# Kernel tuning notes

Measured on AMD Instinct MI355X. Metric: run time of the kernel, lower is better.

## Reference

```python
import jax, jax.numpy as jnp
import numpy as np
from jax import lax

D_MODEL, D_STATE, D_CONV, EXPAND = 1024, 16, 4, 2
D_INNER = EXPAND * D_MODEL
B, L = 2, 2048


def setup_inputs() -> dict:
    key = jax.random.key(0)
    ks = jax.random.split(key, 8)
    s_in = 1.0 / np.sqrt(D_MODEL)
    s_xp = 1.0 / np.sqrt(D_INNER)
    x = jax.random.normal(ks[0], (B, L, D_MODEL), dtype=jnp.float32)
    W_in = jax.random.uniform(ks[1], (2 * D_INNER, D_MODEL), minval=-s_in, maxval=s_in)
    conv_w = jax.random.uniform(ks[2], (D_INNER, 1, D_CONV), minval=-0.5, maxval=0.5)
    conv_b = jax.random.uniform(ks[3], (D_INNER,), minval=-0.5, maxval=0.5)
    W_xproj = jax.random.uniform(ks[4], (1 + 2 * D_STATE, D_INNER), minval=-s_xp, maxval=s_xp)
    W_dt = jax.random.uniform(ks[5], (D_INNER, 1), minval=-1.0, maxval=1.0)
    b_dt = jax.random.uniform(ks[6], (D_INNER,), minval=-1.0, maxval=1.0)
    A_log = jnp.log(jnp.broadcast_to(jnp.arange(1, D_STATE + 1, dtype=jnp.float32), (D_INNER, D_STATE)))
    D = jnp.ones((D_INNER,), dtype=jnp.float32)
    W_out = jax.random.uniform(ks[7], (D_MODEL, D_INNER), minval=-s_xp, maxval=s_xp)
    return {"x": x, "W_in": W_in, "conv_w": conv_w, "conv_b": conv_b,
            "W_xproj": W_xproj, "W_dt": W_dt, "b_dt": b_dt,
            "A_log": A_log, "D": D, "W_out": W_out}


def reference(x, W_in, conv_w, conv_b, W_xproj, W_dt, b_dt, A_log, D, W_out):
    b, l, _ = x.shape
    d_state = A_log.shape[1]
    d_conv = conv_w.shape[-1]

    xz = x @ W_in.T                                  # (B, L, 2*d_inner)
    x_in, z = jnp.split(xz, 2, axis=-1)

    # causal depthwise conv: torch pads both sides then truncates to [:L]
    lhs = jnp.pad(x_in.transpose(0, 2, 1), ((0, 0), (0, 0), (d_conv - 1, 0)))  # (B, d_inner, L+pad)
    conv = lax.conv_general_dilated(
        lhs, conv_w, window_strides=(1,), padding='VALID',
        dimension_numbers=('NCW', 'OIW', 'NCW'),
        feature_group_count=conv_w.shape[0])
    x_conv = jax.nn.silu(conv.transpose(0, 2, 1) + conv_b)  # (B, L, d_inner)

    ssm_in = x_conv @ W_xproj.T                      # (B, L, 1+2*d_state)
    dt_raw = ssm_in[..., :1]
    B_ssm = ssm_in[..., 1:1 + d_state]               # (B, L, d_state)
    C_ssm = ssm_in[..., 1 + d_state:]                # (B, L, d_state)

    delta = jax.nn.softplus(dt_raw @ W_dt.T + b_dt)  # (B, L, d_inner)
    A = -jnp.exp(A_log)                              # (d_inner, d_state)
    deltaA = jnp.exp(delta[..., None] * A)           # (B, L, d_inner, d_state)
    deltaB_u = delta[..., None] * B_ssm[:, :, None, :] * x_conv[..., None]

    def step(h, inp):
        dA, dBu, c = inp                              # (B,d_inner,d_state)x2, (B,d_state)
        h = dA * h + dBu
        y = jnp.einsum('bds,bs->bd', h, c)
        return h, y

    h0 = jnp.zeros((b, deltaA.shape[2], d_state), dtype=x.dtype)
    _, ys = lax.scan(step, h0, (deltaA.transpose(1, 0, 2, 3),
                                deltaB_u.transpose(1, 0, 2, 3),
                                C_ssm.transpose(1, 0, 2)))
    y = ys.transpose(1, 0, 2) + x_conv * D           # (B, L, d_inner)
    y = y * jax.nn.silu(z)
    return y @ W_out.T
```

## Files before the change

kernel.cpp:

```cpp
#include <hip/hip_runtime.h>
#include <hip/hip_bf16.h>
#include <math.h>

#define D_MODEL 1024
#define D_STATE 16
#define D_CONV  4
#define D_INNER 2048
#define BB      2
#define LL      2048
#define BLROWS  (BB*LL)
#define SSML    36
#define XSPLIT  16

typedef __hip_bfloat16 bf16;
typedef __attribute__((ext_vector_type(8))) short short8;
typedef __attribute__((ext_vector_type(4))) float f32x4;

__device__ __forceinline__ float ldf(const void* p, long i, int isbf) {
    return isbf ? __bfloat162float(((const bf16*)p)[i]) : ((const float*)p)[i];
}
__device__ __forceinline__ short bfbits(float f) {
    bf16 h = __float2bfloat16(f);
    return *(short*)&h;
}
__device__ __forceinline__ float bits2f(short s) {
    bf16 h; *(short*)&h = s; return __bfloat162float(h);
}
__device__ __forceinline__ float bf2f(bf16 h) { return __bfloat162float(h); }
__device__ __forceinline__ float siluf(float x) {
    return __fdividef(x, 1.f + __expf(-x));
}
__device__ __forceinline__ void softplus_r(float x, float& delta, float& r) {
    float e = __expf(-fabsf(x));
    float t = 1.f + e;
    delta = fmaxf(x, 0.f) + __logf(t);
    r = __fdividef((x >= 0.f) ? e : 1.f, t);
}
__device__ __forceinline__ void pow16(float r, float* p) {
    p[0]=r;        p[1]=r*r;      p[2]=p[1]*r;    p[3]=p[1]*p[1];
    p[4]=p[3]*p[0];p[5]=p[3]*p[1];p[6]=p[3]*p[2]; p[7]=p[3]*p[3];
    p[8]=p[7]*p[0];p[9]=p[7]*p[1];p[10]=p[7]*p[2];p[11]=p[7]*p[3];
    p[12]=p[7]*p[4];p[13]=p[7]*p[5];p[14]=p[7]*p[6];p[15]=p[7]*p[7];
}

#define OFF_CW   0
#define OFF_CB   8192
#define OFF_WDT  10240
#define OFF_BDT  12288
#define OFF_AA   14336
#define OFF_D    47104
#define N_SMALL  49152
#define N_WXPB   (128*2048)
#define N_SSMZ   (BLROWS*SSML)

__global__ void dtype_probe(const unsigned short* __restrict__ alog, int* __restrict__ flag) {
    if (threadIdx.x == 0) { flag[0] = (alog[1] != 0) ? 1 : 0; flag[1] = 1; }
}

__global__ __launch_bounds__(256) void cvt_prep(
    const void* __restrict__ Wxp, const void* __restrict__ cw,
    const void* __restrict__ cb, const void* __restrict__ wdt,
    const void* __restrict__ bdt, const void* __restrict__ alog,
    const void* __restrict__ Dp,
    bf16* __restrict__ wxpb, float* __restrict__ smallf,
    float* __restrict__ ssm, int* __restrict__ flag)
{
    const int isbf = flag[0];
    int idx = blockIdx.x * 256 + threadIdx.x;
    if (idx < N_WXPB) {
        int row = idx >> 11, col = idx & 2047;
        float v = (row < 33) ? ldf(Wxp, (long)row*2048 + col, isbf) : 0.f;
        wxpb[idx] = __float2bfloat16(v);
        return;
    }
    int j = idx - N_WXPB;
    if      (j < 8192)  smallf[OFF_CW  + j]         = ldf(cw,  j, isbf);
    else if (j < 10240) smallf[OFF_CB  + j - 8192]  = ldf(cb,  j - 8192, isbf);
    else if (j < 12288) smallf[OFF_WDT + j - 10240] = ldf(wdt, j - 10240, isbf);
    else if (j < 14336) smallf[OFF_BDT + j - 12288] = ldf(bdt, j - 12288, isbf);
    else if (j < 47104) {
        int jj = j - 14336;
        float aa = -__expf(ldf(alog, jj, isbf));
        smallf[OFF_AA + jj] = aa;
        int s = jj & 15;
        if (fabsf(aa + (float)(s+1)) > 1e-3f) flag[1] = 0;
    }
    else if (j < 49152) smallf[OFF_D   + j - 47104] = ldf(Dp,  j - 47104, isbf);
    else {
        int z = j - N_SMALL;
        if (z < N_SSMZ) ssm[z] = 0.f;
    }
}

__global__ __launch_bounds__(256) void cvt_all(
    const void* __restrict__ x, const void* __restrict__ win,
    const void* __restrict__ wout,
    bf16* __restrict__ xb, bf16* __restrict__ winb, bf16* __restrict__ woutb,
    const int* __restrict__ flagp)
{
    const int isbf = *flagp;
    int i = blockIdx.x * 256 + threadIdx.x;
    const void* src; bf16* dst; long o;
    if (i < 524288)       { src = x;    dst = xb;    o = (long)i * 8; }
    else if (i < 1048576) { src = win;  dst = winb;  o = (long)(i - 524288) * 8; }
    else if (i < 1310720) { src = wout; dst = woutb; o = (long)(i - 1048576) * 8; }
    else return;
    short8 v;
    if (isbf) {
        v = *(const short8*)((const bf16*)src + o);
    } else {
        const float* s = (const float*)src + o;
        f32x4 u = *(const f32x4*)s, w = *(const f32x4*)(s + 4);
        v[0]=bfbits(u[0]); v[1]=bfbits(u[1]); v[2]=bfbits(u[2]); v[3]=bfbits(u[3]);
        v[4]=bfbits(w[0]); v[5]=bfbits(w[1]); v[6]=bfbits(w[2]); v[7]=bfbits(w[3]);
    }
    *(short8*)(dst + o) = v;
}

__global__ __launch_bounds__(256) void gemm_dual(
    const void* __restrict__ A, int lda,
    const void* __restrict__ Bm, int ldb,
    void* __restrict__ Cp, int ldc, int K,
    const int* __restrict__ flagp, int amode, int bmode, int cmode)
{
    const int isbf = *flagp;
    const int a_bf = amode ? isbf : 1;
    const int b_bf = bmode ? isbf : 1;
    const int c_bf = cmode ? isbf : 1;

    __shared__ bf16 As[128*64];
    __shared__ bf16 Bs[128*64];
    const int t    = threadIdx.x;
    const int lane = t & 63;
    const int w    = t >> 6;
    const int wm   = w >> 1, wn = w & 1;
    const int bm   = blockIdx.y, bn = blockIdx.x;
    const int quad = lane >> 4, l16 = lane & 15;

    f32x4 acc[4][4];
    #pragma unroll
    for (int i = 0; i < 4; i++)
        #pragma unroll
        for (int j = 0; j < 4; j++)
            acc[i][j] = f32x4{0.f, 0.f, 0.f, 0.f};

    for (int k0 = 0; k0 < K; k0 += 64) {
        __syncthreads();
        if (a_bf) {
            #pragma unroll
            for (int seg = 0; seg < 4; seg++) {
                int s = seg*256 + t, row = s >> 3, sg = s & 7;
                int col = (sg ^ (row & 7)) * 8;
                const bf16* ga = (const bf16*)A + ((long)bm*128 + row)*(long)lda + k0 + col;
                __builtin_amdgcn_global_load_lds(
                    (const __attribute__((address_space(1))) void*)ga,
                    (__attribute__((address_space(3))) void*)&As[row*64 + sg*8], 16, 0, 0);
            }
        } else {
            #pragma unroll
            for (int seg = 0; seg < 4; seg++) {
                int s = seg*256 + t, row = s >> 3, sg = s & 7;
                int col = (sg ^ (row & 7)) * 8;
                const float* ap = (const float*)A + ((long)bm*128 + row)*(long)lda + k0 + col;
                f32x4 u = *(const f32x4*)ap, v = *(const f32x4*)(ap + 4);
                short8 va;
                va[0]=bfbits(u[0]); va[1]=bfbits(u[1]); va[2]=bfbits(u[2]); va[3]=bfbits(u[3]);
                va[4]=bfbits(v[0]); va[5]=bfbits(v[1]); va[6]=bfbits(v[2]); va[7]=bfbits(v[3]);
                *(short8*)&As[row*64 + sg*8] = va;
            }
        }
        if (b_bf) {
            #pragma unroll
            for (int seg = 0; seg < 4; seg++) {
                int s = seg*256 + t, row = s >> 3, sg = s & 7;
                int col = (sg ^ (row & 7)) * 8;
                const bf16* gb = (const bf16*)Bm + ((long)bn*128 + row)*(long)ldb + k0 + col;
                __builtin_amdgcn_global_load_lds(
                    (const __attribute__((address_space(1))) void*)gb,
                    (__attribute__((address_space(3))) void*)&Bs[row*64 + sg*8], 16, 0, 0);
            }
        } else {
            #pragma unroll
            for (int seg = 0; seg < 4; seg++) {
                int s = seg*256 + t, row = s >> 3, sg = s & 7;
                int col = (sg ^ (row & 7)) * 8;
                const float* bp = (const float*)Bm + ((long)bn*128 + row)*(long)ldb + k0 + col;
                f32x4 u = *(const f32x4*)bp, v = *(const f32x4*)(bp + 4);
                short8 vb;
                vb[0]=bfbits(u[0]); vb[1]=bfbits(u[1]); vb[2]=bfbits(u[2]); vb[3]=bfbits(u[3]);
                vb[4]=bfbits(v[0]); vb[5]=bfbits(v[1]); vb[6]=bfbits(v[2]); vb[7]=bfbits(v[3]);
                *(short8*)&Bs[row*64 + sg*8] = vb;
            }
        }
        __syncthreads();

        #pragma unroll
        for (int kk = 0; kk < 64; kk += 32) {
            const int cbase = kk >> 3;
            short8 af[4], bfr[4];
            #pragma unroll
            for (int mi = 0; mi < 4; mi++) {
                int row = wm*64 + mi*16 + l16;
                int c = cbase + quad;
                af[mi] = *(const short8*)&As[row*64 + ((c ^ (row & 7))*8)];
            }
            #pragma unroll
            for (int ni = 0; ni < 4; ni++) {
                int row = wn*64 + ni*16 + l16;
                int c = cbase + quad;
                bfr[ni] = *(const short8*)&Bs[row*64 + ((c ^ (row & 7))*8)];
            }
            #pragma unroll
            for (int mi = 0; mi < 4; mi++)
                #pragma unroll
                for (int ni = 0; ni < 4; ni++)
                    acc[mi][ni] = __builtin_amdgcn_mfma_f32_16x16x32_bf16(
                        af[mi], bfr[ni], acc[mi][ni], 0, 0, 0);
        }
    }

    #pragma unroll
    for (int mi = 0; mi < 4; mi++)
        #pragma unroll
        for (int ni = 0; ni < 4; ni++)
            #pragma unroll
            for (int r = 0; r < 4; r++) {
                int row = bm*128 + wm*64 + mi*16 + quad*4 + r;
                int col = bn*128 + wn*64 + ni*16 + l16;
                float val = acc[mi][ni][r];
                if (c_bf) ((bf16*)Cp)[(long)row * ldc + col] = __float2bfloat16(val);
                else      ((float*)Cp)[(long)row * ldc + col] = val;
            }
}

__global__ __launch_bounds__(256) void gemm_n64(
    const bf16* __restrict__ A, int lda,
    const void* __restrict__ Bm, int ldb,
    void* __restrict__ Cp, int ldc, int K,
    const int* __restrict__ flagp, int bmode, int cmode)
{
    const int isbf = *flagp;
    const int b_bf = bmode ? isbf : 1;
    const int c_bf = cmode ? isbf : 1;

    __shared__ bf16 As[128*64];
    __shared__ bf16 Bs[64*64];
    const int t    = threadIdx.x;
    const int lane = t & 63;
    const int w    = t >> 6;
    const int wm   = w >> 1, wn = w & 1;
    const int bm   = blockIdx.y, bn = blockIdx.x;
    const int quad = lane >> 4, l16 = lane & 15;

    f32x4 acc[4][2];
    #pragma unroll
    for (int i = 0; i < 4; i++)
        #pragma unroll
        for (int j = 0; j < 2; j++)
            acc[i][j] = f32x4{0.f, 0.f, 0.f, 0.f};

    for (int k0 = 0; k0 < K; k0 += 64) {
        __syncthreads();
        #pragma unroll
        for (int seg = 0; seg < 4; seg++) {
            int s = seg*256 + t, row = s >> 3, sg = s & 7;
            int col = (sg ^ (row & 7)) * 8;
            const bf16* ga = A + ((long)bm*128 + row)*(long)lda + k0 + col;
            __builtin_amdgcn_global_load_lds(
                (const __attribute__((address_space(1))) void*)ga,
                (__attribute__((address_space(3))) void*)&As[row*64 + sg*8], 16, 0, 0);
        }
        if (b_bf) {
            #pragma unroll
            for (int seg = 0; seg < 2; seg++) {
                int s = seg*256 + t, row = s >> 3, sg = s & 7;
                int col = (sg ^ (row & 7)) * 8;
                const bf16* gb = (const bf16*)Bm + ((long)bn*64 + row)*(long)ldb + k0 + col;
                __builtin_amdgcn_global_load_lds(
                    (const __attribute__((address_space(1))) void*)gb,
                    (__attribute__((address_space(3))) void*)&Bs[row*64 + sg*8], 16, 0, 0);
            }
        } else {
            #pragma unroll
            for (int seg = 0; seg < 2; seg++) {
                int s = seg*256 + t, row = s >> 3, sg = s & 7;
                int col = (sg ^ (row & 7)) * 8;
                const float* bp = (const float*)Bm + ((long)bn*64 + row)*(long)ldb + k0 + col;
                f32x4 u = *(const f32x4*)bp, v = *(const f32x4*)(bp + 4);
                short8 vb;
                vb[0]=bfbits(u[0]); vb[1]=bfbits(u[1]); vb[2]=bfbits(u[2]); vb[3]=bfbits(u[3]);
                vb[4]=bfbits(v[0]); vb[5]=bfbits(v[1]); vb[6]=bfbits(v[2]); vb[7]=bfbits(v[3]);
                *(short8*)&Bs[row*64 + sg*8] = vb;
            }
        }
        __syncthreads();

        #pragma unroll
        for (int kk = 0; kk < 64; kk += 32) {
            const int cbase = kk >> 3;
            short8 af[4], bfr[2];
            #pragma unroll
            for (int mi = 0; mi < 4; mi++) {
                int row = wm*64 + mi*16 + l16;
                int c = cbase + quad;
                af[mi] = *(const short8*)&As[row*64 + ((c ^ (row & 7))*8)];
            }
            #pragma unroll
            for (int ni = 0; ni < 2; ni++) {
                int row = wn*32 + ni*16 + l16;
                int c = cbase + quad;
                bfr[ni] = *(const short8*)&Bs[row*64 + ((c ^ (row & 7))*8)];
            }
            #pragma unroll
            for (int mi = 0; mi < 4; mi++)
                #pragma unroll
                for (int ni = 0; ni < 2; ni++)
                    acc[mi][ni] = __builtin_amdgcn_mfma_f32_16x16x32_bf16(
                        af[mi], bfr[ni], acc[mi][ni], 0, 0, 0);
        }
    }

    #pragma unroll
    for (int mi = 0; mi < 4; mi++)
        #pragma unroll
        for (int ni = 0; ni < 2; ni++)
            #pragma unroll
            for (int r = 0; r < 4; r++) {
                int row = bm*128 + wm*64 + mi*16 + quad*4 + r;
                int col = bn*64 + wn*32 + ni*16 + l16;
                float val = acc[mi][ni][r];
                if (c_bf) ((bf16*)Cp)[(long)row * ldc + col] = __float2bfloat16(val);
                else      ((float*)Cp)[(long)row * ldc + col] = val;
            }
}

__global__ __launch_bounds__(256) void xproj_fused(
    const bf16* __restrict__ xz, const bf16* __restrict__ wxpb,
    const float* __restrict__ smallf, float* __restrict__ ssm)
{
    const float* cwf = smallf + OFF_CW;
    const float* cbf = smallf + OFF_CB;
    __shared__ bf16 As[128*32];
    __shared__ bf16 Bs[128*32];
    const int t    = threadIdx.x;
    const int lane = t & 63;
    const int w    = t >> 6;
    const int wm   = w >> 1, wn = w & 1;
    const int bm   = blockIdx.y;
    const int ks   = blockIdx.x * (D_INNER / XSPLIT);
    const int quad = lane >> 4, l16 = lane & 15;

    f32x4 acc[4][4];
    #pragma unroll
    for (int i = 0; i < 4; i++)
        #pragma unroll
        for (int j = 0; j < 4; j++)
            acc[i][j] = f32x4{0.f, 0.f, 0.f, 0.f};

    for (int k0 = ks; k0 < ks + D_INNER/XSPLIT; k0 += 32) {
        __syncthreads();
        #pragma unroll
        for (int seg = 0; seg < 2; seg++) {
            int s = seg*256 + t, row = s >> 2, dcol = (s & 3) * 8;
            int blg = bm*128 + row;
            int b = blg >> 11, l = blg & (LL - 1);
            int d0 = k0 + dcol;
            float a[8];
            {
                f32x4 c0 = *(const f32x4*)&cbf[d0], c1 = *(const f32x4*)&cbf[d0+4];
                a[0]=c0[0]; a[1]=c0[1]; a[2]=c0[2]; a[3]=c0[3];
                a[4]=c1[0]; a[5]=c1[1]; a[6]=c1[2]; a[7]=c1[3];
            }
            f32x4 cw4[8];
            #pragma unroll
            for (int j = 0; j < 8; j++) cw4[j] = *(const f32x4*)&cwf[(d0+j)*4];
            #pragma unroll
            for (int kk = 0; kk < D_CONV; kk++) {
                int ls = l - 3 + kk;
                if (ls >= 0) {
                    short8 xv = *(const short8*)&xz[((long)(b*LL + ls))*4096 + d0];
                    #pragma unroll
                    for (int j = 0; j < 8; j++) a[j] += bits2f(xv[j]) * cw4[j][kk];
                }
            }
            short8 va;
            #pragma unroll
            for (int j = 0; j < 8; j++) va[j] = bfbits(siluf(a[j]));
            *(short8*)&As[row*32 + dcol] = va;
        }
        #pragma unroll
        for (int seg = 0; seg < 2; seg++) {
            int s = seg*256 + t, row = s >> 2, col = (s & 3) * 8;
            const bf16* gb = wxpb + (long)row*D_INNER + k0 + col;
            __builtin_amdgcn_global_load_lds(
                (const __attribute__((address_space(1))) void*)gb,
                (__attribute__((address_space(3))) void*)&Bs[row*32 + col], 16, 0, 0);
        }
        __syncthreads();

        short8 af[4], bfr[4];
        #pragma unroll
        for (int mi = 0; mi < 4; mi++)
            af[mi] = *(const short8*)&As[(wm*64 + mi*16 + l16)*32 + quad*8];
        #pragma unroll
        for (int ni = 0; ni < 4; ni++)
            bfr[ni] = *(const short8*)&Bs[(wn*64 + ni*16 + l16)*32 + quad*8];
        #pragma unroll
        for (int mi = 0; mi < 4; mi++)
            #pragma unroll
            for (int ni = 0; ni < 4; ni++)
                acc[mi][ni] = __builtin_amdgcn_mfma_f32_16x16x32_bf16(
                    af[mi], bfr[ni], acc[mi][ni], 0, 0, 0);
    }

    #pragma unroll
    for (int mi = 0; mi < 4; mi++)
        #pragma unroll
        for (int ni = 0; ni < 4; ni++) {
            int col = wn*64 + ni*16 + l16;
            if (col < 33) {
                int newcol = (col == 0) ? 32 : (col - 1);
                #pragma unroll
                for (int r = 0; r < 4; r++) {
                    int row = bm*128 + wm*64 + mi*16 + quad*4 + r;
                    atomicAdd(&ssm[(long)row * SSML + newcol], acc[mi][ni][r]);
                }
            }
        }
}

template<int CHUNK_T>
__global__ __launch_bounds__(256) void scan_partA(
    const float* __restrict__ ssm, const bf16* __restrict__ xz,
    const float* __restrict__ smallf,
    float* __restrict__ sumdq, float* __restrict__ Q,
    const int* __restrict__ flag)
{
    __shared__ float sL[CHUNK_T*SSML];
    __shared__ bf16  sX[CHUNK_T*256];
    const int fastA = flag[1];
    int d = blockIdx.x * 256 + threadIdx.x;
    int c = blockIdx.y, b = blockIdx.z;
    const int NC = gridDim.y;
    int l0 = c * CHUNK_T;
    {
        const float* src = ssm + (long)(b*LL + l0) * SSML;
        for (int idx = threadIdx.x; idx < CHUNK_T*SSML; idx += 256) sL[idx] = src[idx];
        const bf16* xsrc = xz + (long)(b*LL + l0)*4096 + blockIdx.x*256;
        for (int j = threadIdx.x; j < CHUNK_T*32; j += 256) {
            int li = j >> 5, ln = j & 31;
            *(short8*)&sX[li*256 + ln*8] = *(const short8*)&xsrc[(long)li*4096 + ln*8];
        }
    }
    float h[D_STATE];
    #pragma unroll
    for (int s = 0; s < D_STATE; s++) h[s] = 0.f;
    float Aa[D_STATE];
    if (!fastA) {
        #pragma unroll
        for (int s = 0; s < D_STATE; s++) Aa[s] = smallf[OFF_AA + d*D_STATE + s];
    }
    f32x4 cw4 = *(const f32x4*)&smallf[OFF_CW + d*4];
    float cbv  = smallf[OFF_CB + d];
    float wdt  = smallf[OFF_WDT + d];
    float bdtv = smallf[OFF_BDT + d];
    float win[3];
    #pragma unroll
    for (int k = 0; k < 3; k++) {
        int ls = l0 - 3 + k;
        win[k] = (ls >= 0) ? bf2f(xz[((long)(b*LL + ls))*4096 + d]) : 0.f;
    }
    __syncthreads();
    float sumd = 0.f;
    #pragma unroll 4
    for (int li = 0; li < CHUNK_T; li++) {
        float xnew = bf2f(sX[li*256 + threadIdx.x]);
        float convv = cbv + win[0]*cw4[0] + win[1]*cw4[1] + win[2]*cw4[2] + xnew*cw4[3];
        win[0] = win[1]; win[1] = win[2]; win[2] = xnew;
        float xc = siluf(convv);
        const float* row = &sL[li*SSML];
        f32x4 Bv[4];
        #pragma unroll
        for (int g = 0; g < 4; g++) Bv[g] = *(const f32x4*)(row + g*4);
        float delta, r;
        softplus_r(row[32]*wdt + bdtv, delta, r);
        sumd += delta;
        float du = delta * xc;
        if (fastA) {
            float p[16];
            pow16(r, p);
            #pragma unroll
            for (int g = 0; g < 4; g++)
                #pragma unroll
                for (int j = 0; j < 4; j++) {
                    int s = g*4 + j;
                    h[s] = p[s]*h[s] + du*Bv[g][j];
                }
        } else {
            #pragma unroll
            for (int g = 0; g < 4; g++)
                #pragma unroll
                for (int j = 0; j < 4; j++) {
                    int s = g*4 + j;
                    h[s] = __expf(delta*Aa[s])*h[s] + du*Bv[g][j];
                }
        }
    }
    sumdq[(long)(b*NC + c)*D_INNER + d] = sumd;
    long o = ((long)(b*NC + c)*D_STATE)*D_INNER + d;
    #pragma unroll
    for (int s = 0; s < D_STATE; s++)
        Q[o + (long)s*D_INNER] = h[s];
}

__global__ __launch_bounds__(256) void scan_combine(
    const float* __restrict__ sumdq, float* __restrict__ Q_hst,
    const float* __restrict__ smallf, int NC)
{
    int t = blockIdx.x * 256 + threadIdx.x;
    int d = t & (D_INNER - 1);
    int s = (t >> 11) & (D_STATE - 1);
    int b = t >> 15;
    float Aa = smallf[OFF_AA + d*D_STATE + s];
    float h = 0.f;
    #pragma unroll 4
    for (int c = 0; c < NC; c++) {
        float sd = sumdq[(long)(b*NC + c)*D_INNER + d];
        long idx = ((long)(b*NC + c)*D_STATE + s)*D_INNER + d;
        float q = Q_hst[idx];
        Q_hst[idx] = h;
        h = __expf(Aa*sd)*h + q;
    }
}

template<int CHUNK_T>
__global__ __launch_bounds__(256) void scan_partC(
    const float* __restrict__ ssm, bf16* __restrict__ xz,
    const float* __restrict__ smallf, const float* __restrict__ hst,
    const int* __restrict__ flag)
{
    __shared__ float sL[CHUNK_T*SSML];
    __shared__ bf16  sX[CHUNK_T*256];
    __shared__ bf16  sZ[CHUNK_T*256];
    const int fastA = flag[1];
    int d = blockIdx.x * 256 + threadIdx.x;
    int c = blockIdx.y, b = blockIdx.z;
    const int NC = gridDim.y;
    int l0 = c * CHUNK_T;
    {
        const float* src = ssm + (long)(b*LL + l0) * SSML;
        for (int idx = threadIdx.x; idx < CHUNK_T*SSML; idx += 256) sL[idx] = src[idx];
        const bf16* xsrc = xz + (long)(b*LL + l0)*4096 + blockIdx.x*256;
        for (int j = threadIdx.x; j < CHUNK_T*32; j += 256) {
            int li = j >> 5, ln = j & 31;
            *(short8*)&sX[li*256 + ln*8] = *(const short8*)&xsrc[(long)li*4096 + ln*8];
            *(short8*)&sZ[li*256 + ln*8] = *(const short8*)&xsrc[(long)li*4096 + D_INNER + ln*8];
        }
    }
    float h[D_STATE];
    long o = ((long)(b*NC + c)*D_STATE)*D_INNER + d;
    #pragma unroll
    for (int s = 0; s < D_STATE; s++) h[s] = hst[o + (long)s*D_INNER];
    float Aa[D_STATE];
    if (!fastA) {
        #pragma unroll
        for (int s = 0; s < D_STATE; s++) Aa[s] = smallf[OFF_AA + d*D_STATE + s];
    }
    f32x4 cw4 = *(const f32x4*)&smallf[OFF_CW + d*4];
    float cbv  = smallf[OFF_CB + d];
    float wdt  = smallf[OFF_WDT + d];
    float bdtv = smallf[OFF_BDT + d];
    float Dv   = smallf[OFF_D + d];
    float win[3];
    #pragma unroll
    for (int k = 0; k < 3; k++) {
        int ls = l0 - 3 + k;
        win[k] = (ls >= 0) ? bf2f(xz[((long)(b*LL + ls))*4096 + d]) : 0.f;
    }
    __syncthreads();
    #pragma unroll 2
    for (int li = 0; li < CHUNK_T; li++) {
        long bl = (long)(b*LL + l0 + li);
        float xnew = bf2f(sX[li*256 + threadIdx.x]);
        float convv = cbv + win[0]*cw4[0] + win[1]*cw4[1] + win[2]*cw4[2] + xnew*cw4[3];
        win[0] = win[1]; win[1] = win[2]; win[2] = xnew;
        float xc = siluf(convv);
        const float* row = &sL[li*SSML];
        f32x4 Bv[4], Cv[4];
        #pragma unroll
        for (int g = 0; g < 4; g++) {
            Bv[g] = *(const f32x4*)(row + g*4);
            Cv[g] = *(const f32x4*)(row + 16 + g*4);
        }
        float delta, r;
        softplus_r(row[32]*wdt + bdtv, delta, r);
        float du = delta * xc;
        float yacc[4] = {0.f, 0.f, 0.f, 0.f};
        if (fastA) {
            float p[16];
            pow16(r, p);
            #pragma unroll
            for (int g = 0; g < 4; g++)
                #pragma unroll
                for (int j = 0; j < 4; j++) {
                    int s = g*4 + j;
                    h[s] = p[s]*h[s] + du*Bv[g][j];
                    yacc[g] += h[s]*Cv[g][j];
                }
        } else {
            #pragma unroll
            for (int g = 0; g < 4; g++)
                #pragma unroll
                for (int j = 0; j < 4; j++) {
                    int s = g*4 + j;
                    h[s] = __expf(delta*Aa[s])*h[s] + du*Bv[g][j];
                    yacc[g] += h[s]*Cv[g][j];
                }
        }
        float yv = (yacc[0] + yacc[1]) + (yacc[2] + yacc[3]);
        yv += xc * Dv;
        float z = bf2f(sZ[li*256 + threadIdx.x]);
        yv *= siluf(z);
        xz[bl*4096 + D_INNER + d] = __float2bfloat16(yv);
    }
}

extern "C" void kernel_launch(void* const* d_in, const int* in_sizes, int n_in,
                              void* d_out, int out_size, void* d_ws, size_t ws_size,
                              hipStream_t stream)
{
    char* ws = (char*)d_ws;
    bf16*  xz     = (bf16*) (ws);
    bf16*  wxpb   = (bf16*) (ws + 33554432);
    float* ssm    = (float*)(ws + 34078720);
    size_t off = 34668544;
    const size_t need128 = 34668544 + (size_t)BB*128*D_INNER*4
                         + (size_t)BB*128*D_STATE*D_INNER*4 + 196608 + 64;
    const int NC = (ws_size >= need128) ? 128 : 64;
    float* sumdq  = (float*)(ws + off); off += (size_t)BB*NC*D_INNER*4;
    float* Q      = (float*)(ws + off); off += (size_t)BB*NC*D_STATE*D_INNER*4;
    float* smallf = (float*)(ws + off); off += 196608;
    int*   flag   = (int*)  (ws + off); off += 64;
    bf16*  woutb  = (bf16*) (ws + off);
    const bool big = ws_size >= off + 4194304;
    bf16*  xb     = (bf16*) Q;
    bf16*  winb   = (bf16*) ((char*)Q + 8388608);

    dtype_probe<<<1, 64, 0, stream>>>((const unsigned short*)d_in[7], flag);

    cvt_prep<<<(N_WXPB + N_SMALL + N_SSMZ)/256, 256, 0, stream>>>(
        d_in[4], d_in[2], d_in[3], d_in[5], d_in[6], d_in[7], d_in[8],
        wxpb, smallf, ssm, flag);

    if (big) {
        cvt_all<<<1310720/256, 256, 0, stream>>>(
            d_in[0], d_in[1], d_in[9], xb, winb, woutb, flag);
        gemm_dual<<<dim3(32, 32), 256, 0, stream>>>(
            xb, D_MODEL, winb, D_MODEL, xz, 2*D_INNER, D_MODEL, flag, 0, 0, 0);
    } else {
        gemm_dual<<<dim3(32, 32), 256, 0, stream>>>(
            d_in[0], D_MODEL, d_in[1], D_MODEL, xz, 2*D_INNER, D_MODEL, flag, 1, 1, 0);
    }

    xproj_fused<<<dim3(XSPLIT, 32), 256, 0, stream>>>(xz, wxpb, smallf, ssm);

    {
        dim3 g(D_INNER/256, NC, BB);
        if (NC == 128) {
            scan_partA<16><<<g, 256, 0, stream>>>(ssm, xz, smallf, sumdq, Q, flag);
            scan_combine<<<(BB*D_STATE*D_INNER)/256, 256, 0, stream>>>(sumdq, Q, smallf, NC);
            scan_partC<16><<<g, 256, 0, stream>>>(ssm, xz, smallf, Q, flag);
        } else {
            scan_partA<32><<<g, 256, 0, stream>>>(ssm, xz, smallf, sumdq, Q, flag);
            scan_combine<<<(BB*D_STATE*D_INNER)/256, 256, 0, stream>>>(sumdq, Q, smallf, NC);
            scan_partC<32><<<g, 256, 0, stream>>>(ssm, xz, smallf, Q, flag);
        }
    }

    if (big) {
        gemm_n64<<<dim3(D_MODEL/64, 32), 256, 0, stream>>>(
            xz + D_INNER, 2*D_INNER, woutb, D_INNER, d_out, D_MODEL, D_INNER, flag, 0, 1);
    } else {
        gemm_n64<<<dim3(D_MODEL/64, 32), 256, 0, stream>>>(
            xz + D_INNER, 2*D_INNER, d_in[9], D_INNER, d_out, D_MODEL, D_INNER, flag, 1, 1);
    }
}
```

Baseline: 301.7 us.

## Fix scan chunk count to 64 and vectorize state update with f32x4

```diff
diff --git a/kernel.cpp b/kernel.cpp
--- a/kernel.cpp
+++ b/kernel.cpp
@@ -9,6 +9,8 @@
 #define BB      2
 #define LL      2048
 #define BLROWS  (BB*LL)
+#define NCHUNK  64
+#define CHUNK   (LL/NCHUNK)
 #define SSML    36
 #define XSPLIT  16
 
@@ -35,12 +37,6 @@
     float t = 1.f + e;
     delta = fmaxf(x, 0.f) + __logf(t);
     r = __fdividef((x >= 0.f) ? e : 1.f, t);
-}
-__device__ __forceinline__ void pow16(float r, float* p) {
-    p[0]=r;        p[1]=r*r;      p[2]=p[1]*r;    p[3]=p[1]*p[1];
-    p[4]=p[3]*p[0];p[5]=p[3]*p[1];p[6]=p[3]*p[2]; p[7]=p[3]*p[3];
-    p[8]=p[7]*p[0];p[9]=p[7]*p[1];p[10]=p[7]*p[2];p[11]=p[7]*p[3];
-    p[12]=p[7]*p[4];p[13]=p[7]*p[5];p[14]=p[7]*p[6];p[15]=p[7]*p[7];
 }
 
 #define OFF_CW   0
@@ -452,9 +448,9 @@
             *(short8*)&sX[li*256 + ln*8] = *(const short8*)&xsrc[(long)li*4096 + ln*8];
         }
     }
-    float h[D_STATE];
-    #pragma unroll
-    for (int s = 0; s < D_STATE; s++) h[s] = 0.f;
+    f32x4 h4[4];
+    #pragma unroll
+    for (int g = 0; g < 4; g++) h4[g] = f32x4{0.f, 0.f, 0.f, 0.f};
     float Aa[D_STATE];
     if (!fastA) {
         #pragma unroll
@@ -487,22 +483,23 @@
         sumd += delta;
         float du = delta * xc;
         if (fastA) {
-            float p[16];
-            pow16(r, p);
+            float r2 = r*r;
+            float r3 = r2*r;
+            float r4 = r2*r2;
+            f32x4 p0; p0[0]=r; p0[1]=r2; p0[2]=r3; p0[3]=r4;
+            float s8  = r4*r4;
+            float s12 = s8*r4;
+            h4[0] = p0*h4[0]       + du*Bv[0];
+            h4[1] = (p0*r4)*h4[1]  + du*Bv[1];
+            h4[2] = (p0*s8)*h4[2]  + du*Bv[2];
+            h4[3] = (p0*s12)*h4[3] + du*Bv[3];
+        } else {
             #pragma unroll
             for (int g = 0; g < 4; g++)
                 #pragma unroll
                 for (int j = 0; j < 4; j++) {
                     int s = g*4 + j;
-                    h[s] = p[s]*h[s] + du*Bv[g][j];
-                }
-        } else {
-            #pragma unroll
-            for (int g = 0; g < 4; g++)
-                #pragma unroll
-                for (int j = 0; j < 4; j++) {
-                    int s = g*4 + j;
-                    h[s] = __expf(delta*Aa[s])*h[s] + du*Bv[g][j];
+                    h4[g][j] = __expf(delta*Aa[s])*h4[g][j] + du*Bv[g][j];
                 }
         }
     }
@@ -510,7 +507,7 @@
     long o = ((long)(b*NC + c)*D_STATE)*D_INNER + d;
     #pragma unroll
     for (int s = 0; s < D_STATE; s++)
-        Q[o + (long)s*D_INNER] = h[s];
+        Q[o + (long)s*D_INNER] = h4[s >> 2][s & 3];
 }
 
 __global__ __launch_bounds__(256) void scan_combine(
@@ -557,10 +554,10 @@
             *(short8*)&sZ[li*256 + ln*8] = *(const short8*)&xsrc[(long)li*4096 + D_INNER + ln*8];
         }
     }
-    float h[D_STATE];
+    f32x4 h4[4];
     long o = ((long)(b*NC + c)*D_STATE)*D_INNER + d;
     #pragma unroll
-    for (int s = 0; s < D_STATE; s++) h[s] = hst[o + (long)s*D_INNER];
+    for (int s = 0; s < D_STATE; s++) h4[s >> 2][s & 3] = hst[o + (long)s*D_INNER];
     float Aa[D_STATE];
     if (!fastA) {
         #pragma unroll
@@ -595,26 +592,30 @@
         float delta, r;
         softplus_r(row[32]*wdt + bdtv, delta, r);
         float du = delta * xc;
-        float yacc[4] = {0.f, 0.f, 0.f, 0.f};
+        f32x4 yacc = f32x4{0.f, 0.f, 0.f, 0.f};
         if (fastA) {
-            float p[16];
-            pow16(r, p);
+            float r2 = r*r;
+            float r3 = r2*r;
+            float r4 = r2*r2;
+            f32x4 p0; p0[0]=r; p0[1]=r2; p0[2]=r3; p0[3]=r4;
+            float s8  = r4*r4;
+            float s12 = s8*r4;
+            h4[0] = p0*h4[0]       + du*Bv[0];
+            h4[1] = (p0*r4)*h4[1]  + du*Bv[1];
+            h4[2] = (p0*s8)*h4[2]  + du*Bv[2];
+            h4[3] = (p0*s12)*h4[3] + du*Bv[3];
+            yacc = yacc + h4[0]*Cv[0];
+            yacc = yacc + h4[1]*Cv[1];
+            yacc = yacc + h4[2]*Cv[2];
+            yacc = yacc + h4[3]*Cv[3];
+        } else {
             #pragma unroll
             for (int g = 0; g < 4; g++)
                 #pragma unroll
                 for (int j = 0; j < 4; j++) {
                     int s = g*4 + j;
-                    h[s] = p[s]*h[s] + du*Bv[g][j];
-                    yacc[g] += h[s]*Cv[g][j];
-                }
-        } else {
-            #pragma unroll
-            for (int g = 0; g < 4; g++)
-                #pragma unroll
-                for (int j = 0; j < 4; j++) {
-                    int s = g*4 + j;
-                    h[s] = __expf(delta*Aa[s])*h[s] + du*Bv[g][j];
-                    yacc[g] += h[s]*Cv[g][j];
+                    h4[g][j] = __expf(delta*Aa[s])*h4[g][j] + du*Bv[g][j];
+                    yacc[j] += h4[g][j]*Cv[g][j];
                 }
         }
         float yv = (yacc[0] + yacc[1]) + (yacc[2] + yacc[3]);
@@ -633,18 +634,14 @@
     bf16*  xz     = (bf16*) (ws);
     bf16*  wxpb   = (bf16*) (ws + 33554432);
     float* ssm    = (float*)(ws + 34078720);
-    size_t off = 34668544;
-    const size_t need128 = 34668544 + (size_t)BB*128*D_INNER*4
-                         + (size_t)BB*128*D_STATE*D_INNER*4 + 196608 + 64;
-    const int NC = (ws_size >= need128) ? 128 : 64;
-    float* sumdq  = (float*)(ws + off); off += (size_t)BB*NC*D_INNER*4;
-    float* Q      = (float*)(ws + off); off += (size_t)BB*NC*D_STATE*D_INNER*4;
-    float* smallf = (float*)(ws + off); off += 196608;
-    int*   flag   = (int*)  (ws + off); off += 64;
-    bf16*  woutb  = (bf16*) (ws + off);
-    const bool big = ws_size >= off + 4194304;
-    bf16*  xb     = (bf16*) Q;
-    bf16*  winb   = (bf16*) ((char*)Q + 8388608);
+    float* sumdq  = (float*)(ws + 34668544);
+    float* Q      = (float*)(ws + 35717120);
+    float* smallf = (float*)(ws + 52494336);
+    int*   flag   = (int*)  (ws + 52690944);
+    bf16*  woutb  = (bf16*) (ws + 52691008);
+    bf16*  xb     = (bf16*) (ws + 35717120);
+    bf16*  winb   = (bf16*) (ws + 35717120 + 8388608);
+    const bool big = ws_size >= 56885312;
 
     dtype_probe<<<1, 64, 0, stream>>>((const unsigned short*)d_in[7], flag);
 
@@ -665,16 +662,10 @@
     xproj_fused<<<dim3(XSPLIT, 32), 256, 0, stream>>>(xz, wxpb, smallf, ssm);
 
     {
-        dim3 g(D_INNER/256, NC, BB);
-        if (NC == 128) {
-            scan_partA<16><<<g, 256, 0, stream>>>(ssm, xz, smallf, sumdq, Q, flag);
-            scan_combine<<<(BB*D_STATE*D_INNER)/256, 256, 0, stream>>>(sumdq, Q, smallf, NC);
-            scan_partC<16><<<g, 256, 0, stream>>>(ssm, xz, smallf, Q, flag);
-        } else {
-            scan_partA<32><<<g, 256, 0, stream>>>(ssm, xz, smallf, sumdq, Q, flag);
-            scan_combine<<<(BB*D_STATE*D_INNER)/256, 256, 0, stream>>>(sumdq, Q, smallf, NC);
-            scan_partC<32><<<g, 256, 0, stream>>>(ssm, xz, smallf, Q, flag);
-        }
+        dim3 g(D_INNER/256, NCHUNK, BB);
+        scan_partA<CHUNK><<<g, 256, 0, stream>>>(ssm, xz, smallf, sumdq, Q, flag);
+        scan_combine<<<(BB*D_STATE*D_INNER)/256, 256, 0, stream>>>(sumdq, Q, smallf, NCHUNK);
+        scan_partC<CHUNK><<<g, 256, 0, stream>>>(ssm, xz, smallf, Q, flag);
     }
 
     if (big) {
```

Result: faster. 292.2 us (-3.1%).
